# Optimization experiments

Hardware: AMD Instinct MI355X
Metric: run time of the kernel (lower is better)

Reference implementation:

```python
import jax, jax.numpy as jnp
import numpy as np
from math import sqrt

HEAD_DIM = 128
MASKED = True


def setup_inputs() -> dict:
    key = jax.random.key(0)
    kq, kk, kv = jax.random.split(key, 3)
    B, S, D = 16, 2048, HEAD_DIM
    return {
        "queries": jax.random.normal(kq, (B, S, D), dtype=jnp.float32),
        "keys": jax.random.normal(kk, (B, S, D), dtype=jnp.float32),
        "values": jax.random.normal(kv, (B, S, D), dtype=jnp.float32),
    }


def reference(queries, keys, values):
    # scores: (B, Sq, Sk)
    scores = jnp.einsum("bqd,bkd->bqk", queries, keys) / sqrt(HEAD_DIM)
    if MASKED:
        # Faithful to torch.tril: upper-triangular entries set to 0.0
        # (NOT -inf) BEFORE softmax — reproduces the original's
        # multiplicative mask semantics exactly.
        scores = jnp.tril(scores)
    weights = jax.nn.softmax(scores, axis=-1)
    return jnp.einsum("bqk,bkd->bqd", weights, values)
```

## Files before the change

### kernel.cpp

```cpp
#include <hip/hip_runtime.h>
#include <hip/hip_bf16.h>

#define DEVI static __device__ __forceinline__

typedef __attribute__((ext_vector_type(8))) short short8;
typedef __attribute__((ext_vector_type(16))) float f32x16;
typedef __attribute__((ext_vector_type(2))) unsigned int uintx2;

#define S_LEN 2048
#define D_DIM 128
#define NBATCH 16
#define QSC ((float)(0.08838834764831845 * 1.4426950408889634))
#define MFIX 8.0f
#define E8 0.00390625f

#if __has_builtin(__builtin_amdgcn_exp2f)
#define EXP2(x) __builtin_amdgcn_exp2f(x)
#else
#define EXP2(x) exp2f(x)
#endif

DEVI unsigned short f2bf(float x) {
  union { float f; unsigned int u; } a; a.f = x;
  unsigned int u = a.u;
  unsigned int r = (u + 0x7fffu + ((u >> 16) & 1u)) >> 16;
  return (unsigned short)r;
}

DEVI unsigned int cvtpk(float lo, float hi) {
  unsigned int r;
  asm volatile("v_cvt_pk_bf16_f32 %0, %1, %2" : "=v"(r) : "v"(lo), "v"(hi));
  return r;
}

DEVI void plswap(unsigned int& a, unsigned int& b) {
  uintx2 r = __builtin_amdgcn_permlane32_swap(a, b, false, false);
  a = r[0];
  b = r[1];
}

DEVI float xhalf_sum(float x) {
  union { float f; unsigned int u; } a, b;
  a.f = x; b.f = x;
  plswap(a.u, b.u);
  return a.f + b.f;
}


__global__ void prep(const float* __restrict__ K, const float* __restrict__ V,
                     unsigned short* __restrict__ Kb, unsigned short* __restrict__ Vt,
                     float* __restrict__ Tsum) {
  __shared__ unsigned short t[64][68];
  const int tt = threadIdx.x;
  if (blockIdx.x >= 1024) {
    const int M4 = (NBATCH * S_LEN * D_DIM) / 4;
    for (int i = (blockIdx.x - 1024) * 256 + tt; i < M4; i += 2048 * 256) {
      const size_t idx = (size_t)i * 4;
      const float4 v = *reinterpret_cast<const float4*>(K + idx);
      ushort4 o;
      o.x = f2bf(v.x); o.y = f2bf(v.y); o.z = f2bf(v.z); o.w = f2bf(v.w);
      *reinterpret_cast<ushort4*>(Kb + idx) = o;
    }
    return;
  }
  const int bid = blockIdx.x;
  const int b = bid >> 6, rem = bid & 63;
  const int st = rem & 31, s0 = st * 64, d0 = (rem >> 5) * 64;
  const int r = tt >> 2, c = (tt & 3) * 16;
  const float* src = V + ((size_t)(b * S_LEN + s0 + r)) * D_DIM + d0 + c;
#pragma unroll
  for (int i = 0; i < 4; i++) {
    float4 v = reinterpret_cast<const float4*>(src)[i];
    t[r][c + 4 * i + 0] = f2bf(v.x);
    t[r][c + 4 * i + 1] = f2bf(v.y);
    t[r][c + 4 * i + 2] = f2bf(v.z);
    t[r][c + 4 * i + 3] = f2bf(v.w);
  }
  __syncthreads();
  unsigned short* dst = Vt + (((size_t)(b * 32 + st)) * 128 + d0 + r) * 64 + c;
#pragma unroll
  for (int i = 0; i < 4; i++) {
    ushort4 o;
    o.x = t[c + 4 * i + 0][r];
    o.y = t[c + 4 * i + 1][r];
    o.z = t[c + 4 * i + 2][r];
    o.w = t[c + 4 * i + 3][r];
    reinterpret_cast<ushort4*>(dst)[i] = o;
  }
  if (tt < 64) {
    float s = 0.0f;
#pragma unroll 8
    for (int rr = 0; rr < 64; rr++) {
      union { float f; unsigned int u; } cv;
      cv.u = ((unsigned int)t[rr][tt]) << 16;
      s += cv.f;
    }
    Tsum[((size_t)b * 32 + st) * 128 + d0 + tt] = s;
  }
}

__global__ void sufB(const float* __restrict__ Tsum, float* __restrict__ SufV) {
  const int b = blockIdx.x;
  const int d = threadIdx.x;
  float v[32];
#pragma unroll
  for (int t = 0; t < 32; t++) v[t] = Tsum[((size_t)b * 32 + t) * 128 + d];
  float run = 0.0f;
  SufV[((size_t)b * 33 + 32) * 128 + d] = 0.0f;
#pragma unroll
  for (int t = 31; t >= 0; t--) {
    run += v[t];
    SufV[((size_t)b * 33 + t) * 128 + d] = run;
  }
}


#define AS1 __attribute__((address_space(1)))
#define AS3 __attribute__((address_space(3)))

DEVI short8 ldK(const char* ldsK, int row, int off) {
  int addr = row * 256 + (off ^ ((row & 15) << 4));
  return *reinterpret_cast<const short8*>(ldsK + addr);
}
DEVI short8 ldV(const char* ldsV, int row, int off) {
  int addr = row * 128 + (off ^ ((row & 7) << 4));
  return *reinterpret_cast<const short8*>(ldsV + addr);
}

template <bool MASK>
DEVI void tile_body(const char* cb, const short8* qf, f32x16 (&acc)[4],
                    float& l_run, const int ln31, const int h, const int kh,
                    const int qrow, const int kvb) {
  f32x16 sT;
#pragma unroll
  for (int r = 0; r < 16; r++) sT[r] = 0.0f;
  __builtin_amdgcn_s_setprio(1);
#pragma unroll
  for (int kf = 0; kf < 8; kf++) {
    short8 af = ldK(cb, ln31 + 32 * kh, 32 * kf + 16 * h);
    sT = __builtin_amdgcn_mfma_f32_32x32x16_bf16(af, qf[kf], sT, 0, 0, 0);
  }
  __builtin_amdgcn_s_setprio(0);
  if (MASK) {
#pragma unroll
    for (int r = 0; r < 16; r++) {
      int kvg = kvb + (r & 3) + 8 * (r >> 2) + 4 * h;
      if (kvg > qrow) sT[r] = 0.0f;
    }
  }
#pragma unroll
  for (int r = 0; r < 16; r++) sT[r] = EXP2(sT[r] - MFIX);
  float ts[8];
#pragma unroll
  for (int r = 0; r < 8; r++) ts[r] = sT[r] + sT[r + 8];
#pragma unroll
  for (int r = 0; r < 4; r++) ts[r] = ts[r] + ts[r + 4];
  float sum = (ts[0] + ts[1]) + (ts[2] + ts[3]);
  sum = xhalf_sum(sum);
  l_run += sum;
#pragma unroll
  for (int kl = 0; kl < 2; kl++) {
    const int ra = 8 * kl;
    const int rb = 8 * kl + 4;
    unsigned int a0 = cvtpk(sT[ra + 0], sT[ra + 1]);
    unsigned int a1 = cvtpk(sT[ra + 2], sT[ra + 3]);
    unsigned int b0 = cvtpk(sT[rb + 0], sT[rb + 1]);
    unsigned int b1 = cvtpk(sT[rb + 2], sT[rb + 3]);
    plswap(a0, b0);
    plswap(a1, b1);
    union { short8 v; unsigned int u[4]; } pa;
    pa.u[0] = a0; pa.u[1] = a1; pa.u[2] = b0; pa.u[3] = b1;
    const int vboff = 64 * kh + 32 * kl + 16 * h;
    __builtin_amdgcn_s_setprio(1);
#pragma unroll
    for (int nt = 0; nt < 4; nt++) {
      short8 vb = ldV(cb + 16384, ln31 + 32 * nt, vboff);
      acc[nt] = __builtin_amdgcn_mfma_f32_32x32x16_bf16(pa.v, vb, acc[nt], 0, 0, 0);
    }
    __builtin_amdgcn_s_setprio(0);
  }
}

#define SMEM_BYTES 66048

__global__ __launch_bounds__(256, 2) void attn_kernel(
    const float* __restrict__ Q, const unsigned short* __restrict__ Kb,
    const unsigned short* __restrict__ Vt, const float* __restrict__ SufV,
    float* __restrict__ out) {
  __shared__ __align__(16) char smem[SMEM_BYTES];

  const int tid = threadIdx.x;
  const int w = tid >> 6, lane = tid & 63;
  const int ln31 = lane & 31, h = lane >> 5;
  const int kh = w & 1;
  const int qh = w >> 1;

  const int bid = blockIdx.x;
  const int x = bid & 7, idx = bid >> 3;
  const int b = 2 * x + (idx & 1);
  const int j = 31 - (idx >> 1);

  const int q0 = j * 64;
  const int kv_end = q0 + 64;
  const int qrow = q0 + 32 * qh + ln31;

  int off[8];
  const char* tbase;
  int dstpart;
  if (w < 2) {
#pragma unroll
    for (int i = 0; i < 8; i++) {
      int L = (w * 8 + i) * 1024 + lane * 16;
      int row = L >> 8;
      off[i] = row * 256 + ((L & 255) ^ ((row & 15) << 4));
    }
    tbase = (const char*)(Kb + (size_t)b * S_LEN * D_DIM);
    dstpart = w * 8192;
  } else {
#pragma unroll
    for (int i = 0; i < 8; i++) {
      int L = ((w - 2) * 8 + i) * 1024 + lane * 16;
      int row = L >> 7;
      off[i] = (L & ~127) + ((L & 127) ^ ((row & 7) << 4));
    }
    tbase = (const char*)Vt + (size_t)b * (S_LEN * D_DIM * 2);
    dstpart = 16384 + (w - 2) * 8192;
  }

#define STAGE(t, bufb)                                                         \
  do {                                                                         \
    const char* src_ = tbase + (size_t)(t) * 16384;                            \
    const int d0_ = (bufb) + dstpart;                                          \
    _Pragma("unroll")                                                          \
    for (int i = 0; i < 8; i++) {                                              \
      __builtin_amdgcn_global_load_lds((const AS1 unsigned int*)(src_ + off[i]),\
                                       (AS3 unsigned int*)(smem + d0_ + i * 1024),\
                                       16, 0, 0);                              \
    }                                                                          \
  } while (0)

  short8 qf[8];
  {
    const float* qsrc = Q + ((size_t)b * S_LEN + qrow) * D_DIM + 8 * h;
#pragma unroll
    for (int kf = 0; kf < 8; kf++) {
      float4 a = *reinterpret_cast<const float4*>(qsrc + 16 * kf);
      float4 d = *reinterpret_cast<const float4*>(qsrc + 16 * kf + 4);
      union { short8 v; unsigned int u[4]; } q8;
      q8.u[0] = cvtpk(a.x * QSC, a.y * QSC);
      q8.u[1] = cvtpk(a.z * QSC, a.w * QSC);
      q8.u[2] = cvtpk(d.x * QSC, d.y * QSC);
      q8.u[3] = cvtpk(d.z * QSC, d.w * QSC);
      qf[kf] = q8.v;
    }
  }

  f32x16 acc[4];
#pragma unroll
  for (int nt = 0; nt < 4; nt++)
#pragma unroll
    for (int rr = 0; rr < 16; rr++) acc[nt][rr] = 0.0f;
  float l_run = 0.0f;

  STAGE(0, 0);
  __syncthreads();
  int buf = 0;
  for (int kt = 0; kt <= j; kt++) {
    const int bb = buf << 15;
    if (kt < j) {
      STAGE(kt + 1, bb ^ 32768);
      tile_body<false>(smem + bb, qf, acc, l_run, ln31, h, kh, qrow,
                       kt * 64 + 32 * kh);
    } else {
      tile_body<true>(smem + bb, qf, acc, l_run, ln31, h, kh, qrow,
                      kt * 64 + 32 * kh);
    }
    __syncthreads();
    buf ^= 1;
  }

  float* pbase = (float*)smem + qh * 4096;
  float* lbase = (float*)(smem + 32768) + qh * 32;
  if (kh == 1) {
#pragma unroll
    for (int nt = 0; nt < 4; nt++)
#pragma unroll
      for (int rr = 0; rr < 16; rr++) {
        int cr = (rr & 3) + 8 * (rr >> 2) + 4 * h;
        pbase[cr * 128 + ln31 + 32 * nt] = acc[nt][rr];
      }
    if (h == 0) lbase[ln31] = l_run;
  }
  __syncthreads();
  if (kh == 0) {
    float l_tot = l_run + lbase[ln31];
    l_tot += (float)(S_LEN - kv_end) * E8;
    const float* sv = SufV + ((size_t)b * 33 + (kv_end >> 6)) * 128;
    float* ob = out + ((size_t)b * S_LEN + q0 + 32 * qh) * D_DIM + ln31;
#pragma unroll
    for (int nt = 0; nt < 4; nt++) {
      float svv = sv[ln31 + 32 * nt];
#pragma unroll
      for (int rr = 0; rr < 16; rr++) {
        int cr = (rr & 3) + 8 * (rr >> 2) + 4 * h;
        float v = acc[nt][rr] + pbase[cr * 128 + ln31 + 32 * nt] + E8 * svv;
        float lq = __shfl(l_tot, cr);
        ob[(size_t)cr * D_DIM + 32 * nt] = v / lq;
      }
    }
  }
}


extern "C" void kernel_launch(void* const* d_in, const int* in_sizes, int n_in,
                              void* d_out, int out_size, void* d_ws, size_t ws_size,
                              hipStream_t stream) {
  const float* Q = (const float*)d_in[0];
  const float* K = (const float*)d_in[1];
  const float* V = (const float*)d_in[2];
  float* out = (float*)d_out;

  char* ws = (char*)d_ws;
  unsigned short* Kb = (unsigned short*)ws;
  unsigned short* Vt = Kb + 4194304;
  float* Tsum = (float*)(ws + 16777216);
  float* SufV = Tsum + 65536;

  prep<<<3072, 256, 0, stream>>>(K, V, Kb, Vt, Tsum);
  sufB<<<16, 128, 0, stream>>>(Tsum, SufV);
  attn_kernel<<<512, 256, 0, stream>>>(Q, Kb, Vt, SufV, out);
}
```

Measured before the change: 62.73 us.

## Drop LDS double buffering to single-buffered K/V tiles with sync

Replaces the double-buffered K/V staging, which prefetched the next tile while computing the current one, with a single 32 KB buffer that is loaded, synchronised, consumed, then synchronised again. The cross-wave l_run reduction is moved to a separate LDS exchange so the epilogue fits in the smaller allocation. Halving LDS use could let more blocks reside per CU, but the load of each tile is no longer overlapped with compute and each iteration now has two barriers.

Result: slower. 66.20 us (+5.5%).

```diff
diff --git a/kernel.cpp b/kernel.cpp
--- a/kernel.cpp
+++ b/kernel.cpp
@@ -181,7 +181,7 @@
   }
 }
 
-#define SMEM_BYTES 66048
+#define SMEM_BYTES 32768
 
 __global__ __launch_bounds__(256, 2) void attn_kernel(
     const float* __restrict__ Q, const unsigned short* __restrict__ Kb,
@@ -227,14 +227,13 @@
     dstpart = 16384 + (w - 2) * 8192;
   }
 
-#define STAGE(t, bufb)                                                         \
+#define STAGE(t)                                                               \
   do {                                                                         \
     const char* src_ = tbase + (size_t)(t) * 16384;                            \
-    const int d0_ = (bufb) + dstpart;                                          \
     _Pragma("unroll")                                                          \
     for (int i = 0; i < 8; i++) {                                              \
       __builtin_amdgcn_global_load_lds((const AS1 unsigned int*)(src_ + off[i]),\
-                                       (AS3 unsigned int*)(smem + d0_ + i * 1024),\
+                                       (AS3 unsigned int*)(smem + dstpart + i * 1024),\
                                        16, 0, 0);                              \
     }                                                                          \
   } while (0)
@@ -262,25 +261,24 @@
     for (int rr = 0; rr < 16; rr++) acc[nt][rr] = 0.0f;
   float l_run = 0.0f;
 
-  STAGE(0, 0);
+  for (int kt = 0; kt <= j; kt++) {
+    STAGE(kt);
+    __syncthreads();
+    if (kt < j)
+      tile_body<false>(smem, qf, acc, l_run, ln31, h, kh, qrow,
+                       kt * 64 + 32 * kh);
+    else
+      tile_body<true>(smem, qf, acc, l_run, ln31, h, kh, qrow,
+                      kt * 64 + 32 * kh);
+    __syncthreads();
+  }
+
+  float* lsh = (float*)smem;
+  if (kh == 1 && h == 0) lsh[qh * 32 + ln31] = l_run;
   __syncthreads();
-  int buf = 0;
-  for (int kt = 0; kt <= j; kt++) {
-    const int bb = buf << 15;
-    if (kt < j) {
-      STAGE(kt + 1, bb ^ 32768);
-      tile_body<false>(smem + bb, qf, acc, l_run, ln31, h, kh, qrow,
-                       kt * 64 + 32 * kh);
-    } else {
-      tile_body<true>(smem + bb, qf, acc, l_run, ln31, h, kh, qrow,
-                      kt * 64 + 32 * kh);
-    }
-    __syncthreads();
-    buf ^= 1;
-  }
-
+  float l_other = lsh[qh * 32 + ln31];
+  __syncthreads();
   float* pbase = (float*)smem + qh * 4096;
-  float* lbase = (float*)(smem + 32768) + qh * 32;
   if (kh == 1) {
 #pragma unroll
     for (int nt = 0; nt < 4; nt++)
@@ -289,12 +287,10 @@
         int cr = (rr & 3) + 8 * (rr >> 2) + 4 * h;
         pbase[cr * 128 + ln31 + 32 * nt] = acc[nt][rr];
       }
-    if (h == 0) lbase[ln31] = l_run;
   }
   __syncthreads();
   if (kh == 0) {
-    float l_tot = l_run + lbase[ln31];
-    l_tot += (float)(S_LEN - kv_end) * E8;
+    float l_tot = l_run + l_other + (float)(S_LEN - kv_end) * E8;
     const float* sv = SufV + ((size_t)b * 33 + (kv_end >> 6)) * 128;
     float* ob = out + ((size_t)b * S_LEN + q0 + 32 * qh) * D_DIM + ln31;
 #pragma unroll
```
